# Kernel tuning notes

Measured on AMD Instinct MI355X. Metric: run time of the kernel, lower is better.

The kernel has to match this reference:

```python
import jax, jax.numpy as jnp
import numpy as np
from jax import lax

N_NODES = 100000
N_EDGES = 3200000
IN_CH = 128
HID = 32
OUT_CH = 64
N_SG = 31  # conv1..conv31, each SGConv(32,32) with K=1 + relu


def setup_inputs() -> dict:
    key = jax.random.key(0)
    ks = jax.random.split(key, 8)
    x = jax.random.normal(ks[0], (N_NODES, IN_CH), dtype=jnp.float32)
    edge_index = jax.random.randint(ks[1], (2, N_EDGES), 0, N_NODES, dtype=jnp.int64)
    s0 = 1.0 / np.sqrt(IN_CH)
    sh = 1.0 / np.sqrt(HID)
    W0 = jax.random.uniform(ks[2], (IN_CH, HID), jnp.float32, -s0, s0)
    b0 = jnp.zeros((HID,), jnp.float32)
    Ws = jax.random.uniform(ks[3], (N_SG, HID, HID), jnp.float32, -sh, sh)
    bs = jnp.zeros((N_SG, HID), jnp.float32)
    W32 = jax.random.uniform(ks[4], (HID, OUT_CH), jnp.float32, -sh, sh)
    b32 = jnp.zeros((OUT_CH,), jnp.float32)
    return {"x": x, "W0": W0, "b0": b0, "Ws": Ws, "bs": bs,
            "W32": W32, "b32": b32, "edge_index": edge_index}


def reference(x, W0, b0, Ws, bs, W32, b32, edge_index):
    N = x.shape[0]
    # GCN normalization with added self-loops (PyG SGConv default, K=1)
    sl = jnp.arange(N, dtype=edge_index.dtype)
    row = jnp.concatenate([edge_index[0], sl])  # source nodes
    col = jnp.concatenate([edge_index[1], sl])  # destination nodes
    deg = jax.ops.segment_sum(jnp.ones(row.shape[0], x.dtype), col, num_segments=N)
    dinv = jnp.where(deg > 0, deg ** -0.5, 0.0)
    norm = dinv[row] * dinv[col]  # [E+N]

    h = x @ W0 + b0  # conv0: plain Linear -> [N, 32]

    def sg_layer(h, wb):
        W, b = wb
        # propagate: D^-1/2 (A+I) D^-1/2 h, then linear + relu
        agg = jax.ops.segment_sum(norm[:, None] * h[row], col, num_segments=N)
        return jax.nn.relu(agg @ W + b), None

    h, _ = lax.scan(sg_layer, h, (Ws, bs))  # conv1..conv31
    return h @ W32 + b32  # conv32: plain Linear -> [N, out_channels]
```

## Files before the change

kernel.cpp:

```cpp
#include <hip/hip_runtime.h>
#include <hip/hip_bf16.h>

#define THREADS 256
#define STRIDE 96
#define CHUNK  4096
#define BSHIFT 9
#define NPB    (1 << BSHIFT)
#define BMAX   512
#define SEG    4096

typedef _Float16 f16;
typedef f16 f16x8 __attribute__((ext_vector_type(8)));
typedef f16 f16x4 __attribute__((ext_vector_type(4)));


__global__ __launch_bounds__(256) void sort_hist_kernel(const int* __restrict__ col,
        int* __restrict__ blockHist, int E, int NBLK, int B) {
    __shared__ int h[BMAX];
    int t = threadIdx.x, blk = blockIdx.x;
    for (int i = t; i < B; i += 256) h[i] = 0;
    __syncthreads();
    int base = blk * CHUNK;
    for (int i = 0; i < CHUNK / 256; ++i) {
        int e = base + i * 256 + t;
        if (e < E) atomicAdd(&h[col[e] >> BSHIFT], 1);
    }
    __syncthreads();
    for (int i = t; i < B; i += 256) blockHist[(size_t)i * NBLK + blk] = h[i];
}

__global__ __launch_bounds__(256) void scan_partial_kernel(const int* __restrict__ a,
        int* __restrict__ segSums, int total) {
    __shared__ int part[256];
    int t = threadIdx.x;
    int base = blockIdx.x * SEG + t * 16;
    int s = 0;
    #pragma unroll
    for (int i = 0; i < 16; ++i) {
        int idx = base + i;
        if (idx < total) s += a[idx];
    }
    part[t] = s;
    __syncthreads();
    for (int off = 128; off > 0; off >>= 1) {
        if (t < off) part[t] += part[t + off];
        __syncthreads();
    }
    if (t == 0) segSums[blockIdx.x] = part[0];
}

__global__ __launch_bounds__(256) void scan_tops_kernel(int* __restrict__ segSums, int G) {
    __shared__ int part[256];
    int t = threadIdx.x;
    int v = (t < G) ? segSums[t] : 0;
    part[t] = v;
    __syncthreads();
    for (int off = 1; off < 256; off <<= 1) {
        int u = (t >= off) ? part[t - off] : 0;
        __syncthreads();
        part[t] += u;
        __syncthreads();
    }
    if (t < G) segSums[t] = part[t] - v;
}

__global__ __launch_bounds__(256) void scan_final_kernel(int* __restrict__ a,
        const int* __restrict__ segSums, int total) {
    __shared__ int part[256];
    int t = threadIdx.x;
    int base = blockIdx.x * SEG + t * 16;
    int v[16];
    int s = 0;
    #pragma unroll
    for (int i = 0; i < 16; ++i) {
        int idx = base + i;
        v[i] = (idx < total) ? a[idx] : 0;
        s += v[i];
    }
    part[t] = s;
    __syncthreads();
    for (int off = 1; off < 256; off <<= 1) {
        int u = (t >= off) ? part[t - off] : 0;
        __syncthreads();
        part[t] += u;
        __syncthreads();
    }
    int run = segSums[blockIdx.x] + part[t] - s;
    #pragma unroll
    for (int i = 0; i < 16; ++i) {
        int idx = base + i;
        if (idx < total) a[idx] = run;
        run += v[i];
    }
}

__global__ __launch_bounds__(256) void sort_scatter_kernel(const int* __restrict__ row,
        const int* __restrict__ col, const int* __restrict__ blockHist,
        int2* __restrict__ ebuf, int E, int NBLK, int B) {
    __shared__ int cur[BMAX];
    int t = threadIdx.x, blk = blockIdx.x;
    for (int i = t; i < B; i += 256) cur[i] = blockHist[(size_t)i * NBLK + blk];
    __syncthreads();
    int base = blk * CHUNK;
    for (int i = 0; i < CHUNK / 256; ++i) {
        int e = base + i * 256 + t;
        if (e < E) {
            int d = col[e];
            int p = atomicAdd(&cur[d >> BSHIFT], 1);
            int2 v; v.x = d; v.y = row[e];
            ebuf[p] = v;
        }
    }
}

__global__ __launch_bounds__(256) void csr_build_kernel(const int2* __restrict__ ebuf,
        const int* __restrict__ blockHist, int* __restrict__ srcs, int* __restrict__ fill,
        int E, int NBLK, int B, int N) {
    __shared__ int cnt[NPB];
    int b = blockIdx.x, t = threadIdx.x;
    for (int i = t; i < NPB; i += 256) cnt[i] = 0;
    __syncthreads();
    int s = blockHist[(size_t)b * NBLK];
    int e = (b + 1 < B) ? blockHist[(size_t)(b + 1) * NBLK] : E;
    for (int i = s + t; i < e; i += 256) {
        int2 ed = ebuf[i];
        int slot = atomicAdd(&cnt[ed.x & (NPB - 1)], 1);
        if (slot < STRIDE) srcs[(size_t)ed.x * STRIDE + slot] = ed.y;
    }
    __syncthreads();
    int nb = b << BSHIFT;
    for (int i = t; i < NPB; i += 256) {
        int node = nb + i;
        if (node < N) fill[node] = cnt[i];
    }
}

__global__ void pad_dinv_kernel(const int* __restrict__ fill, int* __restrict__ srcs,
                                float* __restrict__ dinv, int N) {
    int n = blockIdx.x * blockDim.x + threadIdx.x;
    if (n < N) {
        int d = min(fill[n], STRIDE);
        dinv[n] = 1.0f / sqrtf((float)(d + 1));
        int pd = (d + 7) & ~7;
        int* sp = srcs + (size_t)n * STRIDE;
        for (int j = d; j < pd; ++j) sp[j] = N;
    }
}

__global__ void zrow_kernel(f16* __restrict__ gA, f16* __restrict__ gB, int N) {
    int t = threadIdx.x;
    gA[(size_t)N * 32 + t] = (f16)0.f;
    gB[(size_t)N * 32 + t] = (f16)0.f;
}


__global__ __launch_bounds__(256) void lin0_kernel(const float* __restrict__ x,
        const float* __restrict__ W0, const float* __restrict__ b0,
        const float* __restrict__ dinv, f16* __restrict__ g, int N) {
    __shared__ float Ws[128 * 32];
    int t = threadIdx.x;
    for (int i = t; i < 128 * 32; i += 256) Ws[i] = W0[i];
    __syncthreads();
    int node = blockIdx.x * 32 + (t >> 3);
    int lane = t & 7;
    if (node >= N) return;
    float4 o = ((const float4*)b0)[lane];
    const float* xr = x + (size_t)node * 128;
    for (int k = 0; k < 128; ++k) {
        float a = xr[k];
        float4 w = *(const float4*)&Ws[k * 32 + lane * 4];
        o.x += a * w.x; o.y += a * w.y; o.z += a * w.z; o.w += a * w.w;
    }
    float di = dinv[node];
    f16x4 st;
    st.x = (f16)(o.x * di); st.y = (f16)(o.y * di);
    st.z = (f16)(o.z * di); st.w = (f16)(o.w * di);
    ((f16x4*)g)[(size_t)node * 8 + lane] = st;
}

__global__ __launch_bounds__(256) void sg_layer_kernel(const f16* __restrict__ g_in,
        f16* __restrict__ g_out16, float* __restrict__ h_out32,
        const int* __restrict__ deg, const int* __restrict__ srcs,
        const float* __restrict__ dinv, const float* __restrict__ W,
        const float* __restrict__ b, int N, float bscale, int last) {
    __shared__ float Ws[32 * 32];
    __shared__ float agg[64][33];
    int t = threadIdx.x;
    for (int i = t; i < 32 * 32; i += 256) Ws[i] = W[i];
    int node = blockIdx.x * 64 + (t >> 2);
    int lane = t & 3;
    int ln = t >> 2;
    float o0=0.f,o1=0.f,o2=0.f,o3=0.f,o4=0.f,o5=0.f,o6=0.f,o7=0.f;
    if (node < N) {
        const f16x8* g8 = (const f16x8*)g_in;
        f16x8 sv = g8[(size_t)node * 4 + lane];
        o0=(float)sv[0]; o1=(float)sv[1]; o2=(float)sv[2]; o3=(float)sv[3];
        o4=(float)sv[4]; o5=(float)sv[5]; o6=(float)sv[6]; o7=(float)sv[7];
        int e = node * STRIDE;
        int e1 = e + ((min(deg[node], STRIDE) + 7) & ~7);
        int4 ia, ib;
        if (e < e1) {
            ia = *(const int4*)(srcs + e);
            ib = *(const int4*)(srcs + e + 4);
        }
        while (e < e1) {
            f16x8 v0 = g8[(size_t)ia.x * 4 + lane];
            f16x8 v1 = g8[(size_t)ia.y * 4 + lane];
            f16x8 v2 = g8[(size_t)ia.z * 4 + lane];
            f16x8 v3 = g8[(size_t)ia.w * 4 + lane];
            f16x8 v4 = g8[(size_t)ib.x * 4 + lane];
            f16x8 v5 = g8[(size_t)ib.y * 4 + lane];
            f16x8 v6 = g8[(size_t)ib.z * 4 + lane];
            f16x8 v7 = g8[(size_t)ib.w * 4 + lane];
            e += 8;
            if (e < e1) {
                ia = *(const int4*)(srcs + e);
                ib = *(const int4*)(srcs + e + 4);
            }
            o0 += (((float)v0[0]+(float)v1[0])+((float)v2[0]+(float)v3[0]))
                + (((float)v4[0]+(float)v5[0])+((float)v6[0]+(float)v7[0]));
            o1 += (((float)v0[1]+(float)v1[1])+((float)v2[1]+(float)v3[1]))
                + (((float)v4[1]+(float)v5[1])+((float)v6[1]+(float)v7[1]));
            o2 += (((float)v0[2]+(float)v1[2])+((float)v2[2]+(float)v3[2]))
                + (((float)v4[2]+(float)v5[2])+((float)v6[2]+(float)v7[2]));
            o3 += (((float)v0[3]+(float)v1[3])+((float)v2[3]+(float)v3[3]))
                + (((float)v4[3]+(float)v5[3])+((float)v6[3]+(float)v7[3]));
            o4 += (((float)v0[4]+(float)v1[4])+((float)v2[4]+(float)v3[4]))
                + (((float)v4[4]+(float)v5[4])+((float)v6[4]+(float)v7[4]));
            o5 += (((float)v0[5]+(float)v1[5])+((float)v2[5]+(float)v3[5]))
                + (((float)v4[5]+(float)v5[5])+((float)v6[5]+(float)v7[5]));
            o6 += (((float)v0[6]+(float)v1[6])+((float)v2[6]+(float)v3[6]))
                + (((float)v4[6]+(float)v5[6])+((float)v6[6]+(float)v7[6]));
            o7 += (((float)v0[7]+(float)v1[7])+((float)v2[7]+(float)v3[7]))
                + (((float)v4[7]+(float)v5[7])+((float)v6[7]+(float)v7[7]));
        }
    }
    int c = lane * 8;
    agg[ln][c + 0] = o0; agg[ln][c + 1] = o1; agg[ln][c + 2] = o2; agg[ln][c + 3] = o3;
    agg[ln][c + 4] = o4; agg[ln][c + 5] = o5; agg[ln][c + 6] = o6; agg[ln][c + 7] = o7;
    __syncthreads();
    if (node < N) {
        float4 ma = make_float4(0.f, 0.f, 0.f, 0.f);
        float4 mb = make_float4(0.f, 0.f, 0.f, 0.f);
        for (int k = 0; k < 32; ++k) {
            float a = agg[ln][k];
            float4 wa = *(const float4*)&Ws[k * 32 + c];
            float4 wb = *(const float4*)&Ws[k * 32 + c + 4];
            ma.x += a * wa.x; ma.y += a * wa.y; ma.z += a * wa.z; ma.w += a * wa.w;
            mb.x += a * wb.x; mb.y += a * wb.y; mb.z += a * wb.z; mb.w += a * wb.w;
        }
        float di = dinv[node];
        float4 ba = *(const float4*)&b[c];
        float4 bb = *(const float4*)&b[c + 4];
        float r0 = fmaxf(fmaf(di, ma.x, bscale * ba.x), 0.f);
        float r1 = fmaxf(fmaf(di, ma.y, bscale * ba.y), 0.f);
        float r2 = fmaxf(fmaf(di, ma.z, bscale * ba.z), 0.f);
        float r3 = fmaxf(fmaf(di, ma.w, bscale * ba.w), 0.f);
        float r4 = fmaxf(fmaf(di, mb.x, bscale * bb.x), 0.f);
        float r5 = fmaxf(fmaf(di, mb.y, bscale * bb.y), 0.f);
        float r6 = fmaxf(fmaf(di, mb.z, bscale * bb.z), 0.f);
        float r7 = fmaxf(fmaf(di, mb.w, bscale * bb.w), 0.f);
        if (!last) {
            float sc = 2.0f * di;
            f16x8 st;
            st[0]=(f16)(r0*sc); st[1]=(f16)(r1*sc); st[2]=(f16)(r2*sc); st[3]=(f16)(r3*sc);
            st[4]=(f16)(r4*sc); st[5]=(f16)(r5*sc); st[6]=(f16)(r6*sc); st[7]=(f16)(r7*sc);
            ((f16x8*)g_out16)[(size_t)node * 4 + lane] = st;
        } else {
            const float inv = 1.0f / 1073741824.0f;
            float4 wa = make_float4(r0*inv, r1*inv, r2*inv, r3*inv);
            float4 wb = make_float4(r4*inv, r5*inv, r6*inv, r7*inv);
            float4* hp = (float4*)(h_out32 + (size_t)node * 32 + c);
            hp[0] = wa; hp[1] = wb;
        }
    }
}

__global__ __launch_bounds__(256) void linout_kernel(const float* __restrict__ h,
        const float* __restrict__ W32, const float* __restrict__ b32,
        float* __restrict__ out, int N) {
    __shared__ float Ws[32 * 64];
    int t = threadIdx.x;
    for (int i = t; i < 32 * 64; i += 256) Ws[i] = W32[i];
    __syncthreads();
    int node = blockIdx.x * 16 + (t >> 4);
    int lane = t & 15;
    if (node >= N) return;
    float4 o = ((const float4*)b32)[lane];
    const float* hr = h + (size_t)node * 32;
    for (int k = 0; k < 32; ++k) {
        float a = hr[k];
        float4 w = *(const float4*)&Ws[k * 64 + lane * 4];
        o.x += a * w.x; o.y += a * w.y; o.z += a * w.z; o.w += a * w.w;
    }
    ((float4*)out)[(size_t)node * 16 + lane] = o;
}


extern "C" void kernel_launch(void* const* d_in, const int* in_sizes, int n_in,
                              void* d_out, int out_size, void* d_ws, size_t ws_size,
                              hipStream_t stream) {
    const float* x     = (const float*)d_in[0];
    const float* W0    = (const float*)d_in[1];
    const float* b0    = (const float*)d_in[2];
    const float* Wsall = (const float*)d_in[3];
    const float* bsall = (const float*)d_in[4];
    const float* W32   = (const float*)d_in[5];
    const float* b32   = (const float*)d_in[6];
    const int*   ei    = (const int*)d_in[7];

    const int N   = in_sizes[0] / 128;
    const int E   = in_sizes[7] / 2;
    const int NSG = in_sizes[3] / (32 * 32);
    const int* erow = ei;
    const int* ecol = ei + E;

    const int NBLK  = (E + CHUNK - 1) / CHUNK;
    const int B     = (N + NPB - 1) >> BSHIFT;
    const int total = B * NBLK;
    const int G     = (total + SEG - 1) / SEG;

    char* ws = (char*)d_ws;
    size_t off = 0;
    auto alloc = [&](size_t bytes) { size_t p = off; off += (bytes + 255) & ~(size_t)255; return p; };
    size_t fillOff  = alloc((size_t)N * 4);
    size_t dinvOff  = alloc((size_t)N * 4);
    size_t bhOff    = alloc((size_t)total * 4);
    size_t segOff   = alloc((size_t)G * 4);
    size_t srcsOff  = alloc(((size_t)N * STRIDE + 8) * 4);
    size_t gAOff    = alloc((size_t)(N + 1) * 32 * 2);
    size_t gBOff    = alloc((size_t)(N + 1) * 32 * 2);
    size_t hFOff    = alloc((size_t)N * 32 * 4);

    int*   fill   = (int*)(ws + fillOff);
    float* dinv   = (float*)(ws + dinvOff);
    int*   bh     = (int*)(ws + bhOff);
    int*   seg    = (int*)(ws + segOff);
    int*   srcs   = (int*)(ws + srcsOff);
    f16*   gA     = (f16*)(ws + gAOff);
    f16*   gB     = (f16*)(ws + gBOff);
    float* hF     = (float*)(ws + hFOff);
    int2*  ebuf   = (int2*)(ws + gAOff);

    const int ngrid = (N + THREADS - 1) / THREADS;

    sort_hist_kernel   <<<NBLK, 256, 0, stream>>>(ecol, bh, E, NBLK, B);
    scan_partial_kernel<<<G,    256, 0, stream>>>(bh, seg, total);
    scan_tops_kernel   <<<1,    256, 0, stream>>>(seg, G);
    scan_final_kernel  <<<G,    256, 0, stream>>>(bh, seg, total);
    sort_scatter_kernel<<<NBLK, 256, 0, stream>>>(erow, ecol, bh, ebuf, E, NBLK, B);
    csr_build_kernel   <<<B,    256, 0, stream>>>(ebuf, bh, srcs, fill, E, NBLK, B, N);
    pad_dinv_kernel    <<<ngrid, THREADS, 0, stream>>>(fill, srcs, dinv, N);
    zrow_kernel        <<<1, 32, 0, stream>>>(gA, gB, N);

    lin0_kernel<<<(N + 31) / 32, 256, 0, stream>>>(x, W0, b0, dinv, gA, N);

    f16* cur = gA;
    f16* nxt = gB;
    for (int l = 0; l < NSG; ++l) {
        int last = (l == NSG - 1) ? 1 : 0;
        float bscale = (float)(1u << l);
        sg_layer_kernel<<<(N + 63) / 64, 256, 0, stream>>>(
            cur, nxt, hF, fill, srcs, dinv,
            Wsall + (size_t)l * 32 * 32, bsall + (size_t)l * 32, N, bscale, last);
        f16* tmp = cur; cur = nxt; nxt = tmp;
    }

    linout_kernel<<<(N + 15) / 16, 256, 0, stream>>>(hF, W32, b32, (float*)d_out, N);
}
```

Before: 1.483 ms.

## Pack sorted edges into single ints, fuse padding/dinv into CSR build, larger chunks

The bucket-sorted edge buffer now stores each edge as one 32-bit word (local destination offset in the high 9 bits, source in the low 23 bits) instead of an int2, which halves the scatter write and the CSR-build read traffic. The separate pad/dinv kernel is folded into the CSR build's epilogue, removing one launch and a reread of fill. CHUNK is doubled, which halves the number of sort blocks and the histogram size. The packing assumes source ids fit in 23 bits, which holds for 100k nodes, and the larger chunk may lower parallelism in the hist and scatter kernels.

Measured after the change: 1.482 ms (median of 2 runs). No clear change (-0.1%).

```diff
diff --git a/kernel.cpp b/kernel.cpp
--- a/kernel.cpp
+++ b/kernel.cpp
@@ -3,7 +3,7 @@
 
 #define THREADS 256
 #define STRIDE 96
-#define CHUNK  4096
+#define CHUNK  8192
 #define BSHIFT 9
 #define NPB    (1 << BSHIFT)
 #define BMAX   512
@@ -96,7 +96,7 @@
 
 __global__ __launch_bounds__(256) void sort_scatter_kernel(const int* __restrict__ row,
         const int* __restrict__ col, const int* __restrict__ blockHist,
-        int2* __restrict__ ebuf, int E, int NBLK, int B) {
+        int* __restrict__ ebuf, int E, int NBLK, int B) {
     __shared__ int cur[BMAX];
     int t = threadIdx.x, blk = blockIdx.x;
     for (int i = t; i < B; i += 256) cur[i] = blockHist[(size_t)i * NBLK + blk];
@@ -107,43 +107,39 @@
         if (e < E) {
             int d = col[e];
             int p = atomicAdd(&cur[d >> BSHIFT], 1);
-            int2 v; v.x = d; v.y = row[e];
-            ebuf[p] = v;
-        }
-    }
-}
-
-__global__ __launch_bounds__(256) void csr_build_kernel(const int2* __restrict__ ebuf,
+            ebuf[p] = ((d & (NPB - 1)) << 23) | row[e];
+        }
+    }
+}
+
+__global__ __launch_bounds__(256) void csr_build_kernel(const int* __restrict__ ebuf,
         const int* __restrict__ blockHist, int* __restrict__ srcs, int* __restrict__ fill,
-        int E, int NBLK, int B, int N) {
+        float* __restrict__ dinv, int E, int NBLK, int B, int N) {
     __shared__ int cnt[NPB];
     int b = blockIdx.x, t = threadIdx.x;
     for (int i = t; i < NPB; i += 256) cnt[i] = 0;
     __syncthreads();
     int s = blockHist[(size_t)b * NBLK];
     int e = (b + 1 < B) ? blockHist[(size_t)(b + 1) * NBLK] : E;
+    int nb = b << BSHIFT;
     for (int i = s + t; i < e; i += 256) {
-        int2 ed = ebuf[i];
-        int slot = atomicAdd(&cnt[ed.x & (NPB - 1)], 1);
-        if (slot < STRIDE) srcs[(size_t)ed.x * STRIDE + slot] = ed.y;
-    }
-    __syncthreads();
-    int nb = b << BSHIFT;
+        int v = ebuf[i];
+        int dl = ((unsigned)v) >> 23;
+        int src = v & 0x7FFFFF;
+        int slot = atomicAdd(&cnt[dl], 1);
+        if (slot < STRIDE) srcs[(size_t)(nb + dl) * STRIDE + slot] = src;
+    }
+    __syncthreads();
     for (int i = t; i < NPB; i += 256) {
         int node = nb + i;
-        if (node < N) fill[node] = cnt[i];
-    }
-}
-
-__global__ void pad_dinv_kernel(const int* __restrict__ fill, int* __restrict__ srcs,
-                                float* __restrict__ dinv, int N) {
-    int n = blockIdx.x * blockDim.x + threadIdx.x;
-    if (n < N) {
-        int d = min(fill[n], STRIDE);
-        dinv[n] = 1.0f / sqrtf((float)(d + 1));
-        int pd = (d + 7) & ~7;
-        int* sp = srcs + (size_t)n * STRIDE;
-        for (int j = d; j < pd; ++j) sp[j] = N;
+        if (node < N) {
+            int d = min(cnt[i], STRIDE);
+            fill[node] = d;
+            dinv[node] = 1.0f / sqrtf((float)(d + 1));
+            int pd = (d + 7) & ~7;
+            int* sp = srcs + (size_t)node * STRIDE;
+            for (int j = d; j < pd; ++j) sp[j] = N;
+        }
     }
 }
 
@@ -340,17 +336,14 @@
     f16*   gA     = (f16*)(ws + gAOff);
     f16*   gB     = (f16*)(ws + gBOff);
     float* hF     = (float*)(ws + hFOff);
-    int2*  ebuf   = (int2*)(ws + gAOff);
-
-    const int ngrid = (N + THREADS - 1) / THREADS;
+    int*   ebuf   = (int*)(ws + gAOff);
 
     sort_hist_kernel   <<<NBLK, 256, 0, stream>>>(ecol, bh, E, NBLK, B);
     scan_partial_kernel<<<G,    256, 0, stream>>>(bh, seg, total);
     scan_tops_kernel   <<<1,    256, 0, stream>>>(seg, G);
     scan_final_kernel  <<<G,    256, 0, stream>>>(bh, seg, total);
     sort_scatter_kernel<<<NBLK, 256, 0, stream>>>(erow, ecol, bh, ebuf, E, NBLK, B);
-    csr_build_kernel   <<<B,    256, 0, stream>>>(ebuf, bh, srcs, fill, E, NBLK, B, N);
-    pad_dinv_kernel    <<<ngrid, THREADS, 0, stream>>>(fill, srcs, dinv, N);
+    csr_build_kernel   <<<B,    256, 0, stream>>>(ebuf, bh, srcs, fill, dinv, E, NBLK, B, N);
     zrow_kernel        <<<1, 32, 0, stream>>>(gA, gB, N);
 
     lin0_kernel<<<(N + 31) / 32, 256, 0, stream>>>(x, W0, b0, dinv, gA, N);
```
